# Kernel optimization log

Hardware: AMD Instinct MI355X
Metric: run time of the kernel (lower is better)

Reference implementation:

```python
import jax, jax.numpy as jnp
import numpy as np

INPUT_DIM = 512
OUTPUT_DIM = 512
DEGREE = 7
ALPHA = 0.5


def setup_inputs() -> dict:
    key = jax.random.key(0)
    kx, kc = jax.random.split(key)
    x = jax.random.normal(kx, (8192, INPUT_DIM), dtype=jnp.float32)
    std = 1.0 / (INPUT_DIM * (DEGREE + 1))
    laguerre_coeffs = jax.random.normal(kc, (INPUT_DIM, OUTPUT_DIM, DEGREE + 1), dtype=jnp.float32) * std
    return {"x": x, "laguerre_coeffs": laguerre_coeffs}


def reference(x, laguerre_coeffs):
    # x: [B, I] -> tanh squashed
    xt = jnp.tanh(x.reshape(-1, INPUT_DIM))
    # Build Laguerre basis L_0..L_degree via the standard recurrence:
    # k*L_k = (2(k-1)+1+alpha - x)*L_{k-1} - (k-1+alpha)*L_{k-2}
    L0 = jnp.ones_like(xt)
    basis = [L0]
    if DEGREE > 0:
        L1 = 1.0 + ALPHA - xt
        basis.append(L1)
        Lkm2, Lkm1 = L0, L1
        for k in range(2, DEGREE + 1):
            Lk = ((2 * (k - 1) + 1 + ALPHA - xt) * Lkm1 - (k - 1 + ALPHA) * Lkm2) / k
            basis.append(Lk)
            Lkm2, Lkm1 = Lkm1, Lk
    laguerre = jnp.stack(basis, axis=-1)  # [B, I, D+1]
    y = jnp.einsum('bid,iod->bo', laguerre, laguerre_coeffs)
    return y
```

## Files before the change

kernel.cpp:

```cpp
#include <hip/hip_runtime.h>

#define B_ROWS 8192
#define IN_DIM 512
#define OUT_DIM 512
#define NDEG 8
#define KDIM (IN_DIM * NDEG)
#define ZSLICES 4
#define NKT 16

typedef short bf16x8 __attribute__((ext_vector_type(8)));
typedef float f32x4  __attribute__((ext_vector_type(4)));

__device__ __forceinline__ unsigned short f2bf(float f) {
  unsigned u = __float_as_uint(f);
  u += 0x7fffu + ((u >> 16) & 1u);
  return (unsigned short)(u >> 16);
}

__device__ __forceinline__ void laguerre8(float t, float* L) {
  L[0] = 1.0f;
  L[1] = 1.5f - t;
#pragma unroll
  for (int k = 2; k < NDEG; ++k)
    L[k] = ((2.0f * (float)k - 0.5f - t) * L[k - 1] -
            ((float)k - 0.5f) * L[k - 2]) * (1.0f / (float)k);
}

__device__ __forceinline__ float ftanh(float x) {
  float e2 = __expf(2.0f * x);
  return (e2 - 1.0f) * (1.0f / (e2 + 1.0f));
}

__device__ __forceinline__ uint4 bpack(float xv) {
  float L[NDEG];
  laguerre8(ftanh(xv), L);
  uint4 v;
  v.x = (unsigned)f2bf(L[0]) | ((unsigned)f2bf(L[1]) << 16);
  v.y = (unsigned)f2bf(L[2]) | ((unsigned)f2bf(L[3]) << 16);
  v.z = (unsigned)f2bf(L[4]) | ((unsigned)f2bf(L[5]) << 16);
  v.w = (unsigned)f2bf(L[6]) | ((unsigned)f2bf(L[7]) << 16);
  return v;
}


__global__ void prep_kernel(const float* __restrict__ x, const float* __restrict__ cf,
                            unsigned short* __restrict__ A, unsigned short* __restrict__ Bt) {
  const int g = blockIdx.x, tid = threadIdx.x;
  if (g < 4096) {
    const int h = g >> 6, t = g & 63;
    uint4* dst = (uint4*)A + (size_t)g * 1024;
#pragma unroll
    for (int q = 0; q < 4; ++q) {
      int v = q * 256 + tid;
      int rb = ((v >> 9) << 6) | ((v >> 3) & 63);
      int c = (v & 7) ^ (rb & 7);
      float xv = x[(size_t)(h * 128 + rb) * 512 + t * 8 + c];
      dst[v] = bpack(xv);
    }
  } else {
    int idx = (g - 4096) * 256 + tid;
    int i = idx >> 9, o = idx & 511;
    const float4* cp = (const float4*)(cf + (size_t)idx * 8);
    float4 c0 = cp[0], c1 = cp[1];
    uint4 v;
    v.x = (unsigned)f2bf(c0.x) | ((unsigned)f2bf(c0.y) << 16);
    v.y = (unsigned)f2bf(c0.z) | ((unsigned)f2bf(c0.w) << 16);
    v.z = (unsigned)f2bf(c1.x) | ((unsigned)f2bf(c1.y) << 16);
    v.w = (unsigned)f2bf(c1.z) | ((unsigned)f2bf(c1.w) << 16);
    int h = o >> 7, rb = o & 127, t = i >> 3, c = i & 7;
    size_t chunk = ((size_t)(h * 64 + t)) * 1024 + (rb >> 6) * 512 + (rb & 63) * 8 + (c ^ (rb & 7));
    ((uint4*)Bt)[chunk] = v;
  }
}

#define PH(buf, mq, ks, LOADBF, VMW, ...)                                          \
  {                                                                                \
    const unsigned short* Ab_ = lds + (buf)*16384 + wm*8192 + (mq)*4096 + arow*64; \
    _Pragma("unroll") for (int m4 = 0; m4 < 4; ++m4)                               \
      af[m4] = *(const bf16x8*)(Ab_ + m4*1024 + (e ^ ((ks)*32)));                  \
    if (LOADBF) {                                                                  \
      const unsigned short* Bb_ = lds + 32768 + (buf)*16384 + (wn>>1)*8192         \
                                  + (wn&1)*4096 + arow*64;                         \
      _Pragma("unroll") for (int ni = 0; ni < 4; ++ni)                             \
        bfr[ni] = *(const bf16x8*)(Bb_ + ni*1024 + (e ^ ((ks)*32)));               \
    }                                                                              \
    __VA_ARGS__;                                                                   \
    __builtin_amdgcn_s_barrier();                                                  \
    asm volatile("s_waitcnt lgkmcnt(0)" ::: "memory");                             \
    __builtin_amdgcn_sched_barrier(0);                                             \
    __builtin_amdgcn_s_setprio(1);                                                 \
    _Pragma("unroll") for (int m4 = 0; m4 < 4; ++m4)                               \
      _Pragma("unroll") for (int ni = 0; ni < 4; ++ni)                             \
        acc[(mq)*4+m4][ni] = __builtin_amdgcn_mfma_f32_16x16x32_bf16(              \
            af[m4], bfr[ni], acc[(mq)*4+m4][ni], 0, 0, 0);                         \
    __builtin_amdgcn_s_setprio(0);                                                 \
    if ((VMW) == 1) { asm volatile("s_waitcnt vmcnt(2)" ::: "memory");             \
                      __builtin_amdgcn_sched_barrier(0); }                         \
    if ((VMW) == 2) { asm volatile("s_waitcnt vmcnt(0)" ::: "memory");             \
                      __builtin_amdgcn_sched_barrier(0); }                         \
    __builtin_amdgcn_s_barrier();                                                  \
  }

__global__ __launch_bounds__(512, 2) void gemm_kernel(const unsigned short* __restrict__ A,
                                                      const unsigned short* __restrict__ Bt,
                                                      unsigned short* __restrict__ P) {
  __shared__ unsigned short lds[65536];

  const int tid = threadIdx.x;
  const int lane = tid & 63;
  const int w = tid >> 6;
  const int wm = w >> 2, wn = w & 3;

  const int g = blockIdx.x;
  const int j0 = g >> 3, xx = g & 7;
  const int My = ((j0 >> 3) << 3) | xx;
  const int n = (j0 >> 2) & 1;
  const int z = j0 & 3;

  const uint4* Ag = (const uint4*)A;
  const uint4* Bg = (const uint4*)Bt;

  const int arow = lane & 15, hi = lane >> 4;
  const int e = (hi ^ (arow & 7)) * 8;

  f32x4 zero = {0.f, 0.f, 0.f, 0.f};
  f32x4 acc[8][4];
#pragma unroll
  for (int mi = 0; mi < 8; ++mi)
#pragma unroll
    for (int ni = 0; ni < 4; ++ni) acc[mi][ni] = zero;

  auto STAGE_H = [&](int isB, int h, int tile, int buf) {
    const uint4* src = isB ? Bg : Ag;
    const int rowblk = (isB ? n * 2 : My * 2) + h;
    const size_t c0 = ((size_t)(rowblk * 64 + z * NKT + tile)) * 1024 + w * 64 + lane;
    unsigned short* d = lds + isB * 32768 + buf * 16384 + h * 8192 + w * 512;
    __builtin_amdgcn_global_load_lds(
        (const __attribute__((address_space(1))) unsigned int*)(src + c0),
        (__attribute__((address_space(3))) unsigned int*)d, 16, 0, 0);
    __builtin_amdgcn_global_load_lds(
        (const __attribute__((address_space(1))) unsigned int*)(src + c0 + 512),
        (__attribute__((address_space(3))) unsigned int*)(d + 4096), 16, 0, 0);
  };

  bf16x8 af[4], bfr[4];

  STAGE_H(0, 0, 0, 0); STAGE_H(0, 1, 0, 0);
  STAGE_H(1, 0, 0, 0); STAGE_H(1, 1, 0, 0);
  STAGE_H(1, 0, 1, 1);
  asm volatile("s_waitcnt vmcnt(2)" ::: "memory");
  __builtin_amdgcn_sched_barrier(0);
  __builtin_amdgcn_s_barrier();

  for (int it = 0; it < 7; ++it) {
    const int t1 = 2 * it + 1, t2 = 2 * it + 2, t3 = 2 * it + 3;
    PH(0, 0, 0, 1, 0, STAGE_H(1, 1, t1, 1));
    PH(0, 1, 0, 0, 0, STAGE_H(0, 0, t1, 1));
    PH(0, 0, 1, 1, 0, STAGE_H(0, 1, t1, 1));
    PH(0, 1, 1, 0, 1, STAGE_H(1, 0, t2, 0));
    PH(1, 0, 0, 1, 0, STAGE_H(0, 0, t2, 0));
    PH(1, 1, 0, 0, 0, STAGE_H(0, 1, t2, 0));
    PH(1, 0, 1, 1, 0, STAGE_H(1, 1, t2, 0));
    PH(1, 1, 1, 0, 1, STAGE_H(1, 0, t3, 1));
  }
  PH(0, 0, 0, 1, 0, STAGE_H(1, 1, 15, 1));
  PH(0, 1, 0, 0, 0, STAGE_H(0, 0, 15, 1));
  PH(0, 0, 1, 1, 0, STAGE_H(0, 1, 15, 1));
  PH(0, 1, 1, 0, 2, (void)0);
  PH(1, 0, 0, 1, 0, (void)0);
  PH(1, 1, 0, 0, 0, (void)0);
  PH(1, 0, 1, 1, 0, (void)0);
  PH(1, 1, 1, 0, 0, (void)0);

  unsigned short* W = lds + w * 8192;
#pragma unroll
  for (int mi = 0; mi < 8; ++mi)
#pragma unroll
    for (int ni = 0; ni < 4; ++ni) {
      int col = ni * 16 + arow;
      int c8 = col >> 3, cpos = col & 7;
#pragma unroll
      for (int r = 0; r < 4; ++r) {
        int row = mi * 16 + hi * 4 + r;
        W[row * 64 + ((c8 ^ (row & 7)) << 3) + cpos] = f2bf(acc[mi][ni][r]);
      }
    }
  const int rr = lane >> 3, cc = lane & 7;
#pragma unroll
  for (int it = 0; it < 16; ++it) {
    int row = it * 8 + rr;
    uint4 v = *(uint4*)&W[row * 64 + ((cc ^ (row & 7)) << 3)];
    size_t pr = ((size_t)z * B_ROWS + My * 256 + wm * 128 + row) * 512 + n * 256 + wn * 64 + cc * 8;
    *(uint4*)&P[pr] = v;
  }
}

__global__ void reduce_kernel(const unsigned short* __restrict__ P, float* __restrict__ out) {
  size_t t = (size_t)blockIdx.x * 256 + threadIdx.x;
  const uint4* p = (const uint4*)P;
  const size_t stride = (size_t)B_ROWS * OUT_DIM / 8;
  float s[8] = {0, 0, 0, 0, 0, 0, 0, 0};
#pragma unroll
  for (int zz = 0; zz < ZSLICES; ++zz) {
    uint4 v = p[t + zz * stride];
    unsigned q[4] = {v.x, v.y, v.z, v.w};
#pragma unroll
    for (int j = 0; j < 4; ++j) {
      s[2 * j]     += __uint_as_float((q[j] & 0xffffu) << 16);
      s[2 * j + 1] += __uint_as_float(q[j] & 0xffff0000u);
    }
  }
  float4 o0 = {s[0], s[1], s[2], s[3]}, o1 = {s[4], s[5], s[6], s[7]};
  ((float4*)out)[t * 2]     = o0;
  ((float4*)out)[t * 2 + 1] = o1;
}

__global__ void naive_kernel(const float* __restrict__ x, const float* __restrict__ c,
                             float* __restrict__ out) {
  __shared__ float bas[IN_DIM * NDEG];
  int b = blockIdx.x;
  for (int i = threadIdx.x; i < IN_DIM; i += 256) {
    float t = tanhf(x[(size_t)b * IN_DIM + i]);
    float L[NDEG];
    laguerre8(t, L);
#pragma unroll
    for (int d = 0; d < NDEG; ++d) bas[i * NDEG + d] = L[d];
  }
  __syncthreads();
  for (int o = threadIdx.x; o < OUT_DIM; o += 256) {
    float acc = 0.f;
    for (int i = 0; i < IN_DIM; ++i) {
      const float* cp = c + ((size_t)i * OUT_DIM + o) * NDEG;
#pragma unroll
      for (int d = 0; d < NDEG; ++d) acc += bas[i * NDEG + d] * cp[d];
    }
    out[(size_t)b * OUT_DIM + o] = acc;
  }
}

extern "C" void kernel_launch(void* const* d_in, const int* in_sizes, int n_in,
                              void* d_out, int out_size, void* d_ws, size_t ws_size,
                              hipStream_t stream) {
  const float* x    = (const float*)d_in[0];
  const float* coef = (const float*)d_in[1];
  float* out = (float*)d_out;

  const size_t A_B  = (size_t)B_ROWS * KDIM * 2;
  const size_t P_B  = (size_t)ZSLICES * B_ROWS * OUT_DIM * 2;
  const size_t BT_B = (size_t)OUT_DIM * KDIM * 2;

  if (ws_size >= A_B + P_B + BT_B) {
    unsigned short* Abuf = (unsigned short*)d_ws;
    unsigned short* Pp   = (unsigned short*)((char*)d_ws + A_B);
    unsigned short* Bt   = (unsigned short*)((char*)d_ws + A_B + P_B);
    prep_kernel<<<4096 + 1024, 256, 0, stream>>>(x, coef, Abuf, Bt);
    gemm_kernel<<<256, 512, 0, stream>>>(Abuf, Bt, Pp);
    reduce_kernel<<<(B_ROWS * OUT_DIM / 8) / 256, 256, 0, stream>>>(Pp, out);
  } else {
    naive_kernel<<<B_ROWS, 256, 0, stream>>>(x, coef, out);
  }
}
```

Baseline: 73.77 us.

## Coalesce prep x reads and cut per-phase barriers in GEMM pipeline

Result: faster. 66.66 us (-9.6%).

```diff
diff --git a/kernel.cpp b/kernel.cpp
--- a/kernel.cpp
+++ b/kernel.cpp
@@ -45,20 +45,16 @@
 
 __global__ void prep_kernel(const float* __restrict__ x, const float* __restrict__ cf,
                             unsigned short* __restrict__ A, unsigned short* __restrict__ Bt) {
-  const int g = blockIdx.x, tid = threadIdx.x;
-  if (g < 4096) {
-    const int h = g >> 6, t = g & 63;
-    uint4* dst = (uint4*)A + (size_t)g * 1024;
-#pragma unroll
-    for (int q = 0; q < 4; ++q) {
-      int v = q * 256 + tid;
-      int rb = ((v >> 9) << 6) | ((v >> 3) & 63);
-      int c = (v & 7) ^ (rb & 7);
-      float xv = x[(size_t)(h * 128 + rb) * 512 + t * 8 + c];
-      dst[v] = bpack(xv);
-    }
+  int g = blockIdx.x;
+  if (g < (B_ROWS * IN_DIM) / 256) {
+    int idx = g * 256 + threadIdx.x;
+    int b = idx >> 9, i = idx & 511;
+    uint4 v = bpack(x[idx]);
+    int h = b >> 7, rb = b & 127, t = i >> 3, c = i & 7;
+    size_t chunk = ((size_t)(h * 64 + t)) * 1024 + (rb >> 6) * 512 + (rb & 63) * 8 + (c ^ (rb & 7));
+    ((uint4*)A)[chunk] = v;
   } else {
-    int idx = (g - 4096) * 256 + tid;
+    int idx = (g - (B_ROWS * IN_DIM) / 256) * 256 + threadIdx.x;
     int i = idx >> 9, o = idx & 511;
     const float4* cp = (const float4*)(cf + (size_t)idx * 8);
     float4 c0 = cp[0], c1 = cp[1];
@@ -73,6 +69,7 @@
   }
 }
 
+
 #define PH(buf, mq, ks, LOADBF, VMW, ...)                                          \
   {                                                                                \
     const unsigned short* Ab_ = lds + (buf)*16384 + wm*8192 + (mq)*4096 + arow*64; \
@@ -84,8 +81,8 @@
       _Pragma("unroll") for (int ni = 0; ni < 4; ++ni)                             \
         bfr[ni] = *(const bf16x8*)(Bb_ + ni*1024 + (e ^ ((ks)*32)));               \
     }                                                                              \
-    __VA_ARGS__;                                                                   \
-    __builtin_amdgcn_s_barrier();                                                  \
+    __builtin_amdgcn_s_barrier();             \
+    __VA_ARGS__;                             \
     asm volatile("s_waitcnt lgkmcnt(0)" ::: "memory");                             \
     __builtin_amdgcn_sched_barrier(0);                                             \
     __builtin_amdgcn_s_setprio(1);                                                 \
@@ -95,10 +92,11 @@
             af[m4], bfr[ni], acc[(mq)*4+m4][ni], 0, 0, 0);                         \
     __builtin_amdgcn_s_setprio(0);                                                 \
     if ((VMW) == 1) { asm volatile("s_waitcnt vmcnt(2)" ::: "memory");             \
-                      __builtin_amdgcn_sched_barrier(0); }                         \
+                      __builtin_amdgcn_sched_barrier(0);                           \
+                      __builtin_amdgcn_s_barrier(); }        \
     if ((VMW) == 2) { asm volatile("s_waitcnt vmcnt(0)" ::: "memory");             \
-                      __builtin_amdgcn_sched_barrier(0); }                         \
-    __builtin_amdgcn_s_barrier();                                                  \
+                      __builtin_amdgcn_sched_barrier(0);                           \
+                      __builtin_amdgcn_s_barrier(); }                              \
   }
 
 __global__ __launch_bounds__(512, 2) void gemm_kernel(const unsigned short* __restrict__ A,
@@ -171,6 +169,7 @@
   PH(1, 1, 0, 0, 0, (void)0);
   PH(1, 0, 1, 1, 0, (void)0);
   PH(1, 1, 1, 0, 0, (void)0);
+  __syncthreads();
 
   unsigned short* W = lds + w * 8192;
 #pragma unroll
@@ -253,7 +252,7 @@
     unsigned short* Abuf = (unsigned short*)d_ws;
     unsigned short* Pp   = (unsigned short*)((char*)d_ws + A_B);
     unsigned short* Bt   = (unsigned short*)((char*)d_ws + A_B + P_B);
-    prep_kernel<<<4096 + 1024, 256, 0, stream>>>(x, coef, Abuf, Bt);
+    prep_kernel<<<(B_ROWS * IN_DIM) / 256 + (IN_DIM * OUT_DIM) / 256, 256, 0, stream>>>(x, coef, Abuf, Bt);
     gemm_kernel<<<256, 512, 0, stream>>>(Abuf, Bt, Pp);
     reduce_kernel<<<(B_ROWS * OUT_DIM / 8) / 256, 256, 0, stream>>>(Pp, out);
   } else {
```
